# Kernel tuning notes

Measured on AMD Instinct MI355X. Metric: run time of the kernel, lower is better.

Reference implementation:

```python
import jax, jax.numpy as jnp
import numpy as np

N_NODES = 100000
IN_CH = 128
HIDDEN = 256
N_EDGES = 500000


def setup_inputs() -> dict:
    key = jax.random.key(0)
    k1, k2, k3, k4, k5, k6 = jax.random.split(key, 6)
    latent_space = jax.random.normal(k1, (N_NODES, IN_CH), dtype=jnp.float32)
    edge_index = jax.random.randint(k2, (2, N_EDGES), 0, N_NODES, dtype=jnp.int64)
    # torch Linear params: W is [out, in], y = x @ W.T + b
    lim1 = 1.0 / np.sqrt(2 * IN_CH)
    W1 = jax.random.uniform(k3, (HIDDEN, 2 * IN_CH), minval=-lim1, maxval=lim1, dtype=jnp.float32)
    b1 = jax.random.uniform(k4, (HIDDEN,), minval=-lim1, maxval=lim1, dtype=jnp.float32)
    lim2 = 1.0 / np.sqrt(HIDDEN)
    W2 = jax.random.uniform(k5, (1, HIDDEN), minval=-lim2, maxval=lim2, dtype=jnp.float32)
    b2 = jax.random.uniform(k6, (1,), minval=-lim2, maxval=lim2, dtype=jnp.float32)
    return {"latent_space": latent_space, "W1": W1, "b1": b1, "W2": W2, "b2": b2,
            "edge_index": edge_index}


def reference(latent_space, W1, b1, W2, b2, edge_index):
    src, dst = edge_index[0], edge_index[1]
    h_src = latent_space[src]                      # [E, C]
    h_dst = latent_space[dst]                      # [E, C]
    h_pair = jnp.concatenate([h_src, h_dst], axis=1)  # [E, 2C]
    h = jax.nn.relu(h_pair @ W1.T + b1)            # [E, H]; dropout=0 (eval)
    logits = (h @ W2.T + b2).squeeze(-1)           # [E]
    return jax.nn.sigmoid(logits)
```

## Files before the change

### kernel.cpp

```cpp
#include <hip/hip_runtime.h>
#include <hip/hip_bf16.h>
#include <stdint.h>

#define M_NODES 100000
#define E_EDGES 500000
#define NCOL    512
#define HID     256

typedef unsigned short u16;
typedef u16   u16x8 __attribute__((ext_vector_type(8)));
typedef u16   u16x4 __attribute__((ext_vector_type(4)));
typedef __bf16 bf16x8 __attribute__((ext_vector_type(8)));
typedef float f32x4 __attribute__((ext_vector_type(4)));

static __device__ __forceinline__ u16 f2bf(float f) {
  uint32_t u = __float_as_uint(f);
  u += 0x7fff + ((u >> 16) & 1);
  return (u16)(u >> 16);
}
static __device__ __forceinline__ float bf2f(u16 h) {
  return __uint_as_float(((uint32_t)h) << 16);
}

static __device__ __forceinline__ int col_perm(int p) {
  return (p & ~63) + ((p >> 2) & 3) * 16 + ((p >> 4) & 3) * 4 + (p & 3);
}

__global__ __launch_bounds__(256) void k_weights(const float* __restrict__ W1,
                                                 u16* __restrict__ Bt) {
  int idx = blockIdx.x * 256 + threadIdx.x;
  int j = idx >> 7, k = idx & 127;
  float w = (j < HID) ? W1[j * 256 + k] : W1[(j - HID) * 256 + 128 + k];
  Bt[idx] = f2bf(w);
}

__global__ __launch_bounds__(512, 2) void k_gemm(const float* __restrict__ latent,
                                                 const u16* __restrict__ Bt,
                                                 const float* __restrict__ b1,
                                                 u16* __restrict__ UV) {
  __shared__ __align__(16) u16 ldsA[64 * 128];
  const int t  = threadIdx.x;
  const int w  = t >> 6;
  const int l  = t & 63;
  const int lr = l & 15;
  const int lk = l >> 4;
  const int bm = blockIdx.x;

  bf16x8 fb[4][4];
  {
    const u16* bp = Bt + ((size_t)(w * 64 + lr)) * 128 + lk * 8;
    #pragma unroll
    for (int nt = 0; nt < 4; ++nt)
      #pragma unroll
      for (int ks = 0; ks < 4; ++ks)
        fb[nt][ks] = *reinterpret_cast<const bf16x8*>(bp + nt * 16 * 128 + ks * 32);
  }

  {
    const float4* lat4 = reinterpret_cast<const float4*>(latent);
    #pragma unroll
    for (int i = 0; i < 4; ++i) {
      int idx = i * 512 + t;
      int row = idx >> 5;
      int c4  = idx & 31;
      int grow = bm * 64 + row;
      if (grow >= M_NODES) grow = M_NODES - 1;
      float4 f = lat4[(size_t)grow * 32 + c4];
      u16x4 o;
      o[0] = f2bf(f.x); o[1] = f2bf(f.y); o[2] = f2bf(f.z); o[3] = f2bf(f.w);
      int ss = (c4 >> 1) ^ (row & 7);
      *reinterpret_cast<u16x4*>(&ldsA[row * 128 + ss * 8 + (c4 & 1) * 4]) = o;
    }
  }
  __syncthreads();

  f32x4 acc[4][4];
  #pragma unroll
  for (int i = 0; i < 4; ++i)
    #pragma unroll
    for (int j = 0; j < 4; ++j) acc[i][j] = f32x4{0.f, 0.f, 0.f, 0.f};

  #pragma unroll
  for (int ks = 0; ks < 4; ++ks) {
    bf16x8 fa[4];
    #pragma unroll
    for (int mt = 0; mt < 4; ++mt) {
      int row = mt * 16 + lr;
      int ss  = ((4 * ks + lk) ^ (row & 7));
      fa[mt] = *reinterpret_cast<const bf16x8*>(&ldsA[row * 128 + ss * 8]);
    }
    #pragma unroll
    for (int nt = 0; nt < 4; ++nt)
      #pragma unroll
      for (int mt = 0; mt < 4; ++mt)
        acc[nt][mt] = __builtin_amdgcn_mfma_f32_16x16x32_bf16(fb[nt][ks], fa[mt], acc[nt][mt], 0, 0, 0);
  }

  float b1v[16];
  #pragma unroll
  for (int e = 0; e < 16; ++e) {
    int nt = e >> 2, r = e & 3;
    int n = w * 64 + nt * 16 + lk * 4 + r;
    b1v[e] = (n < HID) ? b1[n] : 0.f;
  }
  #pragma unroll
  for (int mt = 0; mt < 4; ++mt) {
    int mg = bm * 64 + mt * 16 + lr;
    if (mg < M_NODES) {
      u16* dst = &UV[(size_t)mg * NCOL + w * 64 + lk * 16];
      u16x8 o0, o1;
      #pragma unroll
      for (int e = 0; e < 8; ++e) {
        int nt = e >> 2, r = e & 3;
        o0[e] = f2bf(acc[nt][mt][r]     + b1v[e]);
        o1[e] = f2bf(acc[nt + 2][mt][r] + b1v[8 + e]);
      }
      *reinterpret_cast<u16x8*>(dst)     = o0;
      *reinterpret_cast<u16x8*>(dst + 8) = o1;
    }
  }
}

__global__ __launch_bounds__(256, 8) void k_edge(const u16* __restrict__ UV,
                                                 const int* __restrict__ src,
                                                 const int* __restrict__ dst,
                                                 const float* __restrict__ W2,
                                                 const float* __restrict__ b2p,
                                                 float* __restrict__ out) {
  const int t = threadIdx.x;
  const int l = t & 63;
  const int sub = l & 15;
  const int eg = l >> 4;
  const int wid = blockIdx.x * 4 + (t >> 6);
  const int nw = gridDim.x * 4;

  float w2r[16];
  #pragma unroll
  for (int i = 0; i < 16; ++i) w2r[i] = W2[col_perm(sub * 16 + i)];
  const float b2 = *b2p;

  for (int e = wid * 4; e < E_EDGES; e += nw * 4) {
    const int s = src[e + eg];
    const int d = dst[e + eg];
    const u16* pu = UV + (size_t)s * NCOL + sub * 16;
    const u16* pv = UV + (size_t)d * NCOL + HID + sub * 16;
    u16x8 ua = *reinterpret_cast<const u16x8*>(pu);
    u16x8 ub = *reinterpret_cast<const u16x8*>(pu + 8);
    u16x8 va = *reinterpret_cast<const u16x8*>(pv);
    u16x8 vb = *reinterpret_cast<const u16x8*>(pv + 8);
    float a = 0.f;
    #pragma unroll
    for (int i = 0; i < 8; ++i) {
      float h = bf2f(ua[i]) + bf2f(va[i]);
      h = fmaxf(h, 0.f);
      a = fmaf(h, w2r[i], a);
    }
    #pragma unroll
    for (int i = 0; i < 8; ++i) {
      float h = bf2f(ub[i]) + bf2f(vb[i]);
      h = fmaxf(h, 0.f);
      a = fmaf(h, w2r[8 + i], a);
    }
    a += __shfl_xor(a, 1, 64);
    a += __shfl_xor(a, 2, 64);
    a += __shfl_xor(a, 4, 64);
    a += __shfl_xor(a, 8, 64);
    if (sub == 0) {
      out[e + eg] = 1.0f / (1.0f + __expf(-(a + b2)));
    }
  }
}

extern "C" void kernel_launch(void* const* d_in, const int* in_sizes, int n_in,
                              void* d_out, int out_size, void* d_ws, size_t ws_size,
                              hipStream_t stream) {
  const float* latent = (const float*)d_in[0];
  const float* W1     = (const float*)d_in[1];
  const float* b1     = (const float*)d_in[2];
  const float* W2     = (const float*)d_in[3];
  const float* b2     = (const float*)d_in[4];
  const int*   eidx   = (const int*)d_in[5];

  char* ws = (char*)d_ws;
  u16* Btw = (u16*)ws;
  u16* UV  = (u16*)(ws + 131072);

  k_weights<<<256, 256, 0, stream>>>(W1, Btw);
  k_gemm<<<(M_NODES + 63) / 64, 512, 0, stream>>>(latent, Btw, b1, UV);
  k_edge<<<2048, 256, 0, stream>>>(UV, eidx, eidx + E_EDGES, W2, b2, (float*)d_out);
}
```

Baseline: 208.0 us.

## Make node GEMM persistent with double-buffered LDS prefetch; move b1 into edge kernel

The node GEMM becomes a persistent kernel of 512 blocks that loop over row tiles. Each block keeps its W1 fragments in registers across tiles and prefetches the next latent tile into registers while computing the current one, using a double-buffered LDS tile. The b1 bias add moves from the GEMM epilogue to the edge kernel, where it is added after the src and dst halves are summed. This avoids re-reading the weights for every tile and hides latent-load latency. In exchange it adds per-edge adds, and the two-buffer LDS plus the higher occupancy target raise register pressure.

```diff
diff --git a/kernel.cpp b/kernel.cpp
--- a/kernel.cpp
+++ b/kernel.cpp
@@ -6,6 +6,8 @@
 #define E_EDGES 500000
 #define NCOL    512
 #define HID     256
+#define NTILES  ((M_NODES + 63) / 64)
+#define GGEMM   512
 
 typedef unsigned short u16;
 typedef u16   u16x8 __attribute__((ext_vector_type(8)));
@@ -34,17 +36,15 @@
   Bt[idx] = f2bf(w);
 }
 
-__global__ __launch_bounds__(512, 2) void k_gemm(const float* __restrict__ latent,
+__global__ __launch_bounds__(512, 4) void k_gemm(const float* __restrict__ latent,
                                                  const u16* __restrict__ Bt,
-                                                 const float* __restrict__ b1,
                                                  u16* __restrict__ UV) {
-  __shared__ __align__(16) u16 ldsA[64 * 128];
+  __shared__ __align__(16) u16 ldsA[2][64 * 128];
   const int t  = threadIdx.x;
   const int w  = t >> 6;
   const int l  = t & 63;
   const int lr = l & 15;
   const int lk = l >> 4;
-  const int bm = blockIdx.x;
 
   bf16x8 fb[4][4];
   {
@@ -56,68 +56,99 @@
         fb[nt][ks] = *reinterpret_cast<const bf16x8*>(bp + nt * 16 * 128 + ks * 32);
   }
 
-  {
-    const float4* lat4 = reinterpret_cast<const float4*>(latent);
+  const int row_ = t >> 5;
+  const int c4_  = t & 31;
+  const float4* lat4 = reinterpret_cast<const float4*>(latent);
+
+  float4 st[4];
+
+  int tile = blockIdx.x;
+  if (tile >= NTILES) return;
+
+  #pragma unroll
+  for (int i = 0; i < 4; ++i) {
+    int row = i * 16 + row_;
+    int grow = tile * 64 + row;
+    if (grow >= M_NODES) grow = M_NODES - 1;
+    st[i] = lat4[(size_t)grow * 32 + c4_];
+  }
+  #pragma unroll
+  for (int i = 0; i < 4; ++i) {
+    int row = i * 16 + row_;
+    u16x4 o;
+    o[0] = f2bf(st[i].x); o[1] = f2bf(st[i].y); o[2] = f2bf(st[i].z); o[3] = f2bf(st[i].w);
+    int ss = (c4_ >> 1) ^ (row & 7);
+    *reinterpret_cast<u16x4*>(&ldsA[0][row * 128 + ss * 8 + (c4_ & 1) * 4]) = o;
+  }
+
+  int cur = 0;
+  while (true) {
+    const int nxt = tile + GGEMM;
+    const bool has = (nxt < NTILES);
+
+    if (has) {
+      #pragma unroll
+      for (int i = 0; i < 4; ++i) {
+        int row = i * 16 + row_;
+        int grow = nxt * 64 + row;
+        if (grow >= M_NODES) grow = M_NODES - 1;
+        st[i] = lat4[(size_t)grow * 32 + c4_];
+      }
+    }
+
+    __syncthreads();
+
+    f32x4 acc[4][4];
+    #pragma unroll
+    for (int i = 0; i < 4; ++i)
+      #pragma unroll
+      for (int j = 0; j < 4; ++j) acc[i][j] = f32x4{0.f, 0.f, 0.f, 0.f};
+
+    #pragma unroll
+    for (int ks = 0; ks < 4; ++ks) {
+      bf16x8 fa[4];
+      #pragma unroll
+      for (int mt = 0; mt < 4; ++mt) {
+        int row = mt * 16 + lr;
+        int ss  = ((4 * ks + lk) ^ (row & 7));
+        fa[mt] = *reinterpret_cast<const bf16x8*>(&ldsA[cur][row * 128 + ss * 8]);
+      }
+      #pragma unroll
+      for (int nt = 0; nt < 4; ++nt)
+        #pragma unroll
+        for (int mt = 0; mt < 4; ++mt)
+          acc[nt][mt] = __builtin_amdgcn_mfma_f32_16x16x32_bf16(fb[nt][ks], fa[mt], acc[nt][mt], 0, 0, 0);
+    }
+
+    #pragma unroll
+    for (int mt = 0; mt < 4; ++mt) {
+      int mg = tile * 64 + mt * 16 + lr;
+      if (mg < M_NODES) {
+        u16* dst = &UV[(size_t)mg * NCOL + w * 64 + lk * 16];
+        u16x8 o0, o1;
+        #pragma unroll
+        for (int e = 0; e < 8; ++e) {
+          int nt = e >> 2, r = e & 3;
+          o0[e] = f2bf(acc[nt][mt][r]);
+          o1[e] = f2bf(acc[nt + 2][mt][r]);
+        }
+        *reinterpret_cast<u16x8*>(dst)     = o0;
+        *reinterpret_cast<u16x8*>(dst + 8) = o1;
+      }
+    }
+
+    if (!has) break;
+
     #pragma unroll
     for (int i = 0; i < 4; ++i) {
-      int idx = i * 512 + t;
-      int row = idx >> 5;
-      int c4  = idx & 31;
-      int grow = bm * 64 + row;
-      if (grow >= M_NODES) grow = M_NODES - 1;
-      float4 f = lat4[(size_t)grow * 32 + c4];
+      int row = i * 16 + row_;
       u16x4 o;
-      o[0] = f2bf(f.x); o[1] = f2bf(f.y); o[2] = f2bf(f.z); o[3] = f2bf(f.w);
-      int ss = (c4 >> 1) ^ (row & 7);
-      *reinterpret_cast<u16x4*>(&ldsA[row * 128 + ss * 8 + (c4 & 1) * 4]) = o;
-    }
-  }
-  __syncthreads();
-
-  f32x4 acc[4][4];
-  #pragma unroll
-  for (int i = 0; i < 4; ++i)
-    #pragma unroll
-    for (int j = 0; j < 4; ++j) acc[i][j] = f32x4{0.f, 0.f, 0.f, 0.f};
-
-  #pragma unroll
-  for (int ks = 0; ks < 4; ++ks) {
-    bf16x8 fa[4];
-    #pragma unroll
-    for (int mt = 0; mt < 4; ++mt) {
-      int row = mt * 16 + lr;
-      int ss  = ((4 * ks + lk) ^ (row & 7));
-      fa[mt] = *reinterpret_cast<const bf16x8*>(&ldsA[row * 128 + ss * 8]);
-    }
-    #pragma unroll
-    for (int nt = 0; nt < 4; ++nt)
-      #pragma unroll
-      for (int mt = 0; mt < 4; ++mt)
-        acc[nt][mt] = __builtin_amdgcn_mfma_f32_16x16x32_bf16(fb[nt][ks], fa[mt], acc[nt][mt], 0, 0, 0);
-  }
-
-  float b1v[16];
-  #pragma unroll
-  for (int e = 0; e < 16; ++e) {
-    int nt = e >> 2, r = e & 3;
-    int n = w * 64 + nt * 16 + lk * 4 + r;
-    b1v[e] = (n < HID) ? b1[n] : 0.f;
-  }
-  #pragma unroll
-  for (int mt = 0; mt < 4; ++mt) {
-    int mg = bm * 64 + mt * 16 + lr;
-    if (mg < M_NODES) {
-      u16* dst = &UV[(size_t)mg * NCOL + w * 64 + lk * 16];
-      u16x8 o0, o1;
-      #pragma unroll
-      for (int e = 0; e < 8; ++e) {
-        int nt = e >> 2, r = e & 3;
-        o0[e] = f2bf(acc[nt][mt][r]     + b1v[e]);
-        o1[e] = f2bf(acc[nt + 2][mt][r] + b1v[8 + e]);
-      }
-      *reinterpret_cast<u16x8*>(dst)     = o0;
-      *reinterpret_cast<u16x8*>(dst + 8) = o1;
-    }
+      o[0] = f2bf(st[i].x); o[1] = f2bf(st[i].y); o[2] = f2bf(st[i].z); o[3] = f2bf(st[i].w);
+      int ss = (c4_ >> 1) ^ (row & 7);
+      *reinterpret_cast<u16x4*>(&ldsA[cur ^ 1][row * 128 + ss * 8 + (c4_ & 1) * 4]) = o;
+    }
+    cur ^= 1;
+    tile = nxt;
   }
 }
 
@@ -125,6 +156,7 @@
                                                  const int* __restrict__ src,
                                                  const int* __restrict__ dst,
                                                  const float* __restrict__ W2,
+                                                 const float* __restrict__ b1,
                                                  const float* __restrict__ b2p,
                                                  float* __restrict__ out) {
   const int t = threadIdx.x;
@@ -134,9 +166,13 @@
   const int wid = blockIdx.x * 4 + (t >> 6);
   const int nw = gridDim.x * 4;
 
-  float w2r[16];
+  float w2r[16], b1r[16];
   #pragma unroll
-  for (int i = 0; i < 16; ++i) w2r[i] = W2[col_perm(sub * 16 + i)];
+  for (int i = 0; i < 16; ++i) {
+    int lc = col_perm(sub * 16 + i);
+    w2r[i] = W2[lc];
+    b1r[i] = b1[lc];
+  }
   const float b2 = *b2p;
 
   for (int e = wid * 4; e < E_EDGES; e += nw * 4) {
@@ -151,13 +187,13 @@
     float a = 0.f;
     #pragma unroll
     for (int i = 0; i < 8; ++i) {
-      float h = bf2f(ua[i]) + bf2f(va[i]);
+      float h = bf2f(ua[i]) + bf2f(va[i]) + b1r[i];
       h = fmaxf(h, 0.f);
       a = fmaf(h, w2r[i], a);
     }
     #pragma unroll
     for (int i = 0; i < 8; ++i) {
-      float h = bf2f(ub[i]) + bf2f(vb[i]);
+      float h = bf2f(ub[i]) + bf2f(vb[i]) + b1r[8 + i];
       h = fmaxf(h, 0.f);
       a = fmaf(h, w2r[8 + i], a);
     }
@@ -186,6 +222,6 @@
   u16* UV  = (u16*)(ws + 131072);
 
   k_weights<<<256, 256, 0, stream>>>(W1, Btw);
-  k_gemm<<<(M_NODES + 63) / 64, 512, 0, stream>>>(latent, Btw, b1, UV);
-  k_edge<<<2048, 256, 0, stream>>>(UV, eidx, eidx + E_EDGES, W2, b2, (float*)d_out);
-}
+  k_gemm<<<GGEMM, 512, 0, stream>>>(latent, Btw, UV);
+  k_edge<<<2048, 256, 0, stream>>>(UV, eidx, eidx + E_EDGES, W2, b1, b2, (float*)d_out);
+}
```

After: 259.6 us. 1.25x slower.
